# Optimization experiments

Measured on AMD Instinct MI355X. Metric: run time of the kernel, lower is better.

Reference implementation:

```python
import jax, jax.numpy as jnp
import numpy as np

EPS = 1e-10
REG = 1e-6  # regularization_weight passed to sparse_image_warp


def _phi(r2):
    # order-2 polyharmonic (thin-plate) kernel: 0.5 * r^2 * log(r^2)
    return 0.5 * r2 * jnp.log(jnp.maximum(r2, EPS))


def _tps_interpolate(train_pts, train_vals, query_pts, reg):
    # train_pts: (B,N,2), train_vals: (B,N,2), query_pts: (B,Q,2)
    b, n, _ = train_pts.shape
    d2 = jnp.sum((train_pts[:, :, None, :] - train_pts[:, None, :, :]) ** 2, -1)
    A = _phi(d2) + reg * jnp.eye(n, dtype=train_pts.dtype)  # (B,N,N)
    ones_n = jnp.ones((b, n, 1), train_pts.dtype)
    Bm = jnp.concatenate([train_pts, ones_n], -1)  # (B,N,3)
    top = jnp.concatenate([A, Bm], -1)
    bot = jnp.concatenate([jnp.swapaxes(Bm, 1, 2), jnp.zeros((b, 3, 3), train_pts.dtype)], -1)
    lhs = jnp.concatenate([top, bot], 1)  # (B,N+3,N+3)
    rhs = jnp.concatenate([train_vals, jnp.zeros((b, 3, train_vals.shape[-1]), train_vals.dtype)], 1)
    sol = jnp.linalg.solve(lhs, rhs)
    w, v = sol[:, :n], sol[:, n:]  # rbf weights (B,N,2), affine (B,3,2)
    q2 = jnp.sum((query_pts[:, :, None, :] - train_pts[:, None, :, :]) ** 2, -1)  # (B,Q,N)
    rbf = jnp.einsum('bqn,bnd->bqd', _phi(q2), w)
    ones_q = jnp.ones((b, query_pts.shape[1], 1), query_pts.dtype)
    lin = jnp.einsum('bqk,bkd->bqd', jnp.concatenate([query_pts, ones_q], -1), v)
    return rbf + lin


def _bilinear_sample(image, qy, qx):
    # image: (B,H,W,C); qy,qx: (B,Q) float query coordinates (TF dense_image_warp clamping)
    B, H, W, C = image.shape
    y0 = jnp.clip(jnp.floor(qy), 0, H - 2).astype(jnp.int32)
    x0 = jnp.clip(jnp.floor(qx), 0, W - 2).astype(jnp.int32)
    ay = jnp.clip(qy - y0.astype(qy.dtype), 0.0, 1.0)[..., None]
    ax = jnp.clip(qx - x0.astype(qx.dtype), 0.0, 1.0)[..., None]
    bi = jnp.arange(B)[:, None]
    g = lambda yi, xi: image[bi, yi, xi]  # gather -> (B,Q,C)
    top = g(y0, x0) * (1 - ax) + g(y0, x0 + 1) * ax
    bot = g(y0 + 1, x0) * (1 - ax) + g(y0 + 1, x0 + 1) * ax
    return top * (1 - ay) + bot * ay


def _sparse_image_warp(image, src, dst, reg):
    # TF semantics: flows at control points = dst - src, interpolated at dst; sample at grid - flow
    B, H, W, C = image.shape
    flows_ctrl = dst - src  # (B,N,2)
    gy, gx = jnp.meshgrid(jnp.arange(H, dtype=image.dtype), jnp.arange(W, dtype=image.dtype), indexing='ij')
    grid = jnp.broadcast_to(jnp.stack([gy, gx], -1).reshape(1, H * W, 2), (B, H * W, 2))
    dense_flow = _tps_interpolate(dst, flows_ctrl, grid, reg)  # (B,HW,2)
    query = grid - dense_flow
    warped = _bilinear_sample(image, query[..., 0], query[..., 1])
    return warped.reshape(B, H, W, C), dense_flow.reshape(B, H, W, 2)


def setup_inputs() -> dict:
    key = jax.random.key(0)
    ks = jax.random.split(key, 8)
    B, C, H, W = 16, 64, 112, 112
    n_ldmark = 16
    F = C * H * W
    x = jax.random.normal(ks[0], (B, C, H, W), jnp.float32)
    images_rendered = jax.random.normal(ks[1], (B, H, W, C), jnp.float32)
    scales = jax.random.uniform(ks[2], (B, 1), jnp.float32)
    W1 = jax.random.normal(ks[3], (128, F), jnp.float32) / np.float32(np.sqrt(F))
    b1 = jnp.zeros((128,), jnp.float32)
    W2 = jax.random.normal(ks[4], (n_ldmark * 2, 128), jnp.float32) / np.float32(np.sqrt(128))
    b2 = jnp.zeros((n_ldmark * 2,), jnp.float32)
    W3 = jax.random.normal(ks[5], (n_ldmark * 2, 128), jnp.float32) / np.float32(np.sqrt(128))
    b3 = jnp.zeros((n_ldmark * 2,), jnp.float32)
    # torch.normal(mean=0, std=50, size=(n_ldmark,2)) + [0.5*H, 0.5*W], fixed for determinism
    landmarks_mean = jax.random.normal(ks[6], (n_ldmark, 2), jnp.float32) * 50.0 \
        + jnp.array([0.5 * H, 0.5 * W], jnp.float32)
    return {"x": x, "images_rendered": images_rendered, "scales": scales,
            "W1": W1, "b1": b1, "W2": W2, "b2": b2, "W3": W3, "b3": b3,
            "landmarks_mean": landmarks_mean}


def reference(x, images_rendered, scales, W1, b1, W2, b2, W3, b3, landmarks_mean):
    B = x.shape[0]
    n_ldmark = landmarks_mean.shape[0]
    feat = x.reshape(B, -1)
    out = feat @ W1.T + b1  # (B,128)
    landmarks_pred = out @ W2.T + b2 + landmarks_mean.reshape(-1)  # (B, 2*n_ldmark)
    landmarks_disp = (out @ W3.T + b3) * scales
    # original uses .detach().clone() on landmark coords -> stop_gradient
    src = jax.lax.stop_gradient(landmarks_pred).reshape(B, n_ldmark, 2)
    dst = jax.lax.stop_gradient(landmarks_pred + landmarks_disp).reshape(B, n_ldmark, 2)
    # torch.norm(..., dim=(1,2)) = per-batch Frobenius norm, then mean
    landmarks_norm = jnp.mean(jnp.sqrt(jnp.sum((src - dst) ** 2, axis=(1, 2))))
    warped, _dense_flow = _sparse_image_warp(images_rendered, src, dst, REG)
    images_transformed = jnp.transpose(warped, (0, 3, 1, 2))  # NHWC -> NCHW
    return images_transformed, landmarks_pred, landmarks_norm
```

## Files before the change

### kernel.cpp

```cpp
#include <hip/hip_runtime.h>
#include <math.h>
#include <stdint.h>

#define F_K 802816
#define KC 1024
#define NB1 784
#define PRED_OFF 12845056
#define NORM_OFF 12845568

#define AS3 __attribute__((address_space(3)))
#define AS1 __attribute__((address_space(1)))

__device__ __forceinline__ void gload16(const float* gsrc, float* ldsbase) {
  __builtin_amdgcn_global_load_lds((const AS1 uint32_t*)gsrc, (AS3 uint32_t*)ldsbase, 16, 0, 0);
}
__device__ __forceinline__ void gload16_nt(const float* gsrc, float* ldsbase) {
  __builtin_amdgcn_global_load_lds((const AS1 uint32_t*)gsrc, (AS3 uint32_t*)ldsbase, 16, 0, 2);
}

__global__ __launch_bounds__(256) void k_gemm1(const float* __restrict__ x,
                                               const float* __restrict__ w1,
                                               float* __restrict__ part) {
  __shared__ __align__(16) float xs[256 * 4];
  __shared__ __align__(16) float ws[2048 * 4];
  const int t = threadIdx.x;
  const int wave = t >> 6, lane = t & 63;
  const int nl = t & 15;
  const int bg = (t >> 4) & 3;
  const size_t k0 = (size_t)blockIdx.x * KC;

  const float* wsrc[8];
#pragma unroll
  for (int cc = 0; cc < 8; ++cc) {
    int f = cc * 64 + lane;
    int n = f >> 2, tau = f & 3;
    int q = (tau - (n >> 1)) & 3;
    wsrc[cc] = w1 + (size_t)n * F_K + k0 + 16 * wave + 4 * q;
  }
  const float* xsrc;
  {
    int b = lane >> 2, tau = lane & 3;
    int q = (tau - (b >> 1)) & 3;
    xsrc = x + (size_t)b * F_K + k0 + 16 * wave + 4 * q;
  }
  float* xbase = xs + wave * 256;
  float* wbase = ws + wave * 2048;

  float acc[4][8];
#pragma unroll
  for (int i = 0; i < 4; ++i)
#pragma unroll
    for (int j = 0; j < 8; ++j) acc[i][j] = 0.f;

  for (int kt = 0; kt < KC / 64; ++kt) {
    asm volatile("s_waitcnt lgkmcnt(0)" ::: "memory");
    gload16(xsrc + kt * 64, xbase);
#pragma unroll
    for (int cc = 0; cc < 8; ++cc) gload16_nt(wsrc[cc] + kt * 64, wbase + cc * 256);
    asm volatile("s_waitcnt vmcnt(0)" ::: "memory");
    __builtin_amdgcn_sched_barrier(0);
#pragma unroll
    for (int q = 0; q < 4; ++q) {
      float4 xv[4];
#pragma unroll
      for (int i = 0; i < 4; ++i) {
        int b = 4 * bg + i;
        int tx = (q + (b >> 1)) & 3;
        xv[i] = *reinterpret_cast<const float4*>(&xbase[b * 16 + 4 * tx]);
      }
      const int tw = (q + (nl >> 1)) & 3;
#pragma unroll
      for (int j = 0; j < 8; ++j) {
        float4 wv = *reinterpret_cast<const float4*>(&wbase[(16 * j + nl) * 16 + 4 * tw]);
#pragma unroll
        for (int i = 0; i < 4; ++i) {
          acc[i][j] += xv[i].x * wv.x;
          acc[i][j] += xv[i].y * wv.y;
          acc[i][j] += xv[i].z * wv.z;
          acc[i][j] += xv[i].w * wv.w;
        }
      }
    }
  }

  __syncthreads();
  float* red = ws;
#pragma unroll
  for (int i = 0; i < 4; ++i)
#pragma unroll
    for (int j = 0; j < 8; ++j)
      red[wave * 2048 + (4 * bg + i) * 128 + 16 * j + nl] = acc[i][j];
  __syncthreads();
  const int o8 = t * 8;
  float4 s0 = {0, 0, 0, 0}, s1 = {0, 0, 0, 0};
#pragma unroll
  for (int w = 0; w < 4; ++w) {
    float4 a = *reinterpret_cast<const float4*>(&red[w * 2048 + o8]);
    float4 b = *reinterpret_cast<const float4*>(&red[w * 2048 + o8 + 4]);
    s0.x += a.x; s0.y += a.y; s0.z += a.z; s0.w += a.w;
    s1.x += b.x; s1.y += b.y; s1.z += b.z; s1.w += b.w;
  }
  float* pp = part + (size_t)blockIdx.x * 2048 + o8;
  *reinterpret_cast<float4*>(pp) = s0;
  *reinterpret_cast<float4*>(pp + 4) = s1;
}

__global__ __launch_bounds__(256) void k_red(const float* __restrict__ part,
                                             float* __restrict__ p2) {
  int pc = blockIdx.x >> 3, ib = blockIdx.x & 7;
  int idx = ib * 256 + threadIdx.x;
  const float* p = part + (size_t)pc * 49 * 2048 + idx;
  float s = 0.f;
  for (int q = 0; q < 49; ++q) s += p[(size_t)q * 2048];
  p2[pc * 2048 + idx] = s;
}

__global__ __launch_bounds__(64) void k_small(const float* __restrict__ p2,
    const float* __restrict__ b1, const float* __restrict__ W2, const float* __restrict__ b2,
    const float* __restrict__ W3, const float* __restrict__ b3,
    const float* __restrict__ lmean, const float* __restrict__ scales,
    float* __restrict__ dout_pred, float* __restrict__ coef, float* __restrict__ norms) {
  const int b = blockIdx.x, lane = threadIdx.x;
  __shared__ float o[128], dflat[32], fl[32], A[19][22], farr[19], sol[19][2];

  for (int h = 0; h < 2; ++h) {
    int n = lane + 64 * h;
    float s = b1[n];
    for (int pc = 0; pc < 16; ++pc) s += p2[pc * 2048 + b * 128 + n];
    o[n] = s;
  }
  __syncthreads();

  const int j = lane & 31;
  const float* Wm = (lane < 32) ? (W2 + j * 128) : (W3 + j * 128);
  float acc = 0.f;
#pragma unroll 4
  for (int n = 0; n < 128; ++n) acc += o[n] * Wm[n];
  float other = __shfl(acc, j + 32);
  float sc = scales[b];
  float dspv = 0.f;
  if (lane < 32) {
    float predv = acc + b2[j] + lmean[j];
    dspv = (other + b3[j]) * sc;
    dout_pred[b * 32 + j] = predv;
    dflat[j] = predv + dspv;
    fl[j] = dspv;
  }
  float s2 = (lane < 32) ? dspv * dspv : 0.f;
  for (int off = 32; off; off >>= 1) s2 += __shfl_xor(s2, off);
  if (lane == 0) norms[b] = sqrtf(s2);
  __syncthreads();

  for (int cell = lane; cell < 19 * 21; cell += 64) {
    int r = cell / 21, cc = cell - (cell / 21) * 21;
    float v;
    if (r < 16) {
      if (cc < 16) {
        float dy = dflat[2*r] - dflat[2*cc], dx = dflat[2*r+1] - dflat[2*cc+1];
        float d2 = dy * dy + dx * dx;
        v = 0.5f * d2 * logf(fmaxf(d2, 1e-10f));
        if (r == cc) v += 1e-6f;
      } else if (cc == 16) v = dflat[2*r];
      else if (cc == 17) v = dflat[2*r+1];
      else if (cc == 18) v = 1.0f;
      else if (cc == 19) v = fl[2*r];
      else               v = fl[2*r+1];
    } else {
      int rr = r - 16;
      if (cc < 16) v = (rr == 0) ? dflat[2*cc] : (rr == 1) ? dflat[2*cc+1] : 1.0f;
      else         v = 0.0f;
    }
    A[r][cc] = v;
  }
  __syncthreads();

  for (int k = 0; k < 19; ++k) {
    float av = (lane >= k && lane < 19) ? fabsf(A[lane][k]) : -1.0f;
    int idx = lane;
    for (int off = 32; off; off >>= 1) {
      float v2 = __shfl_xor(av, off);
      int  i2 = __shfl_xor(idx, off);
      if (v2 > av) { av = v2; idx = i2; }
    }
    idx = __shfl(idx, 0);
    if (idx != k && lane < 21) {
      float tmp = A[k][lane]; A[k][lane] = A[idx][lane]; A[idx][lane] = tmp;
    }
    __syncthreads();
    float invp = 1.0f / A[k][k];
    if (lane < 19) farr[lane] = (lane > k) ? A[lane][k] * invp : 0.0f;
    __syncthreads();
    int nr = 18 - k, nc = 20 - k;
    for (int cell = lane; cell < nr * nc; cell += 64) {
      int i = k + 1 + cell / nc, jj = k + 1 + cell % nc;
      A[i][jj] -= farr[i] * A[k][jj];
    }
    __syncthreads();
  }
  for (int k = 18; k >= 0; --k) {
    if (lane < 2) sol[k][lane] = A[k][19 + lane] / A[k][k];
    __syncthreads();
    if (lane < 2 * k) {
      int i = lane >> 1, cc = lane & 1;
      A[i][19 + cc] -= A[i][k] * sol[k][cc];
    }
    __syncthreads();
  }
  float* cf = coef + b * 80;
  if (lane < 32) { cf[lane] = sol[lane >> 1][lane & 1]; cf[38 + lane] = dflat[lane]; }
  else if (lane < 38) cf[lane] = sol[16 + ((lane - 32) >> 1)][(lane - 32) & 1];
}

__global__ __launch_bounds__(256) void k_warp(const float* __restrict__ img,
                                              const float* __restrict__ coef,
                                              const float* __restrict__ norms,
                                              float* __restrict__ out) {
  const int bid = blockIdx.x;
  const int b = bid / 112, y = bid - (bid / 112) * 112;
  const int t = threadIdx.x;
  __shared__ float qy[112], qx[112];
  __shared__ float cw[32], cv[6], cd[32];
  __shared__ float tile[64][113];

  if (bid == 0 && t == 0) {
    float s = 0.f;
    for (int i = 0; i < 16; ++i) s += norms[i];
    out[NORM_OFF] = s * (1.0f / 16.0f);
  }
  const float* cf = coef + b * 80;
  if (t < 70) {
    float v = cf[t];
    if (t < 32) cw[t] = v;
    else if (t < 38) cv[t - 32] = v;
    else cd[t - 38] = v;
  }
  __syncthreads();

  if (t < 112) {
    float fy = (float)y, fx = (float)t;
    float s0 = cv[0] * fy + cv[2] * fx + cv[4];
    float s1 = cv[1] * fy + cv[3] * fx + cv[5];
#pragma unroll
    for (int i = 0; i < 16; ++i) {
      float dy = fy - cd[2 * i], dx = fx - cd[2 * i + 1];
      float d2 = dy * dy + dx * dx;
      float ph = 0.5f * d2 * logf(fmaxf(d2, 1e-10f));
      s0 += ph * cw[2 * i];
      s1 += ph * cw[2 * i + 1];
    }
    qy[t] = fy - s0;
    qx[t] = fx - s1;
  }
  __syncthreads();

  const int wave = t >> 6, lane = t & 63;
#pragma unroll 4
  for (int p = 0; p < 28; ++p) {
    int xx = wave * 28 + p;
    float fy = qy[xx], fx = qx[xx];
    float y0f = fminf(fmaxf(floorf(fy), 0.f), 110.f);
    float x0f = fminf(fmaxf(floorf(fx), 0.f), 110.f);
    float ay = fminf(fmaxf(fy - y0f, 0.f), 1.f);
    float ax = fminf(fmaxf(fx - x0f, 0.f), 1.f);
    int y0 = (int)y0f, x0 = (int)x0f;
    const float* p00 = img + (((size_t)(b * 112 + y0) * 112 + x0) * 64) + lane;
    float v00 = p00[0], v01 = p00[64];
    float v10 = p00[112 * 64], v11 = p00[112 * 64 + 64];
    float top = v00 * (1.f - ax) + v01 * ax;
    float bot = v10 * (1.f - ax) + v11 * ax;
    tile[lane][xx] = top * (1.f - ay) + bot * ay;
  }
  __syncthreads();

  float* ob = out + (size_t)b * 64 * 12544 + y * 112;
  for (int i = 0; i < 28; ++i) {
    int idx = i * 256 + t;
    int cc = idx / 112, xx = idx - cc * 112;
    ob[(size_t)cc * 12544 + xx] = tile[cc][xx];
  }
}

extern "C" void kernel_launch(void* const* d_in, const int* in_sizes, int n_in,
                              void* d_out, int out_size, void* d_ws, size_t ws_size,
                              hipStream_t stream) {
  const float* x      = (const float*)d_in[0];
  const float* img    = (const float*)d_in[1];
  const float* scales = (const float*)d_in[2];
  const float* W1     = (const float*)d_in[3];
  const float* b1     = (const float*)d_in[4];
  const float* W2     = (const float*)d_in[5];
  const float* b2     = (const float*)d_in[6];
  const float* W3     = (const float*)d_in[7];
  const float* b3     = (const float*)d_in[8];
  const float* lmean  = (const float*)d_in[9];
  float* out = (float*)d_out;
  float* ws  = (float*)d_ws;

  float* P1   = ws;
  float* P2   = P1 + (size_t)NB1 * 2048;
  float* COEF = P2 + 16 * 2048;
  float* NORM = COEF + 16 * 80;

  k_gemm1<<<NB1, 256, 0, stream>>>(x, W1, P1);
  k_red  <<<128, 256, 0, stream>>>(P1, P2);
  k_small<<<16, 64, 0, stream>>>(P2, b1, W2, b2, W3, b3, lmean, scales,
                                 out + PRED_OFF, COEF, NORM);
  k_warp <<<16 * 112, 256, 0, stream>>>(img, COEF, NORM, out);
}
```

Baseline: 216.3 us.

## Split GEMM1 tile by output columns per wave with shared x tile and shuffle reduction

The first GEMM kernel now assigns each wave 32 output neurons across all 16 batch rows, instead of splitting K across waves. The block loads one shared 16x64 x tile, replacing per-wave x copies, and reduces partial sums across the K sub-lanes with cross-lane shuffles instead of an LDS reduction over four waves. This removes the block-level LDS reduction and the extra LDS traffic, but adds two __syncthreads per K step and drops the non-temporal load hint on W1. Per-lane reads of x from LDS become broadcast-heavy (16 float4 loads per kk step).

Result: faster. 198.6 us (-8.2%).

```diff
diff --git a/kernel.cpp b/kernel.cpp
--- a/kernel.cpp
+++ b/kernel.cpp
@@ -14,95 +14,74 @@
 __device__ __forceinline__ void gload16(const float* gsrc, float* ldsbase) {
   __builtin_amdgcn_global_load_lds((const AS1 uint32_t*)gsrc, (AS3 uint32_t*)ldsbase, 16, 0, 0);
 }
-__device__ __forceinline__ void gload16_nt(const float* gsrc, float* ldsbase) {
-  __builtin_amdgcn_global_load_lds((const AS1 uint32_t*)gsrc, (AS3 uint32_t*)ldsbase, 16, 0, 2);
-}
 
 __global__ __launch_bounds__(256) void k_gemm1(const float* __restrict__ x,
                                                const float* __restrict__ w1,
                                                float* __restrict__ part) {
-  __shared__ __align__(16) float xs[256 * 4];
-  __shared__ __align__(16) float ws[2048 * 4];
+  __shared__ __align__(16) float xs[16 * 64];
+  __shared__ __align__(16) float wsd[4 * 2048];
   const int t = threadIdx.x;
   const int wave = t >> 6, lane = t & 63;
-  const int nl = t & 15;
-  const int bg = (t >> 4) & 3;
+  const int nl = lane & 15, h = lane >> 4;
+  const int rs = lane >> 4;
+  const int ss = lane & 15;
   const size_t k0 = (size_t)blockIdx.x * KC;
 
   const float* wsrc[8];
 #pragma unroll
   for (int cc = 0; cc < 8; ++cc) {
-    int f = cc * 64 + lane;
-    int n = f >> 2, tau = f & 3;
-    int q = (tau - (n >> 1)) & 3;
-    wsrc[cc] = w1 + (size_t)n * F_K + k0 + 16 * wave + 4 * q;
-  }
-  const float* xsrc;
-  {
-    int b = lane >> 2, tau = lane & 3;
-    int q = (tau - (b >> 1)) & 3;
-    xsrc = x + (size_t)b * F_K + k0 + 16 * wave + 4 * q;
-  }
-  float* xbase = xs + wave * 256;
-  float* wbase = ws + wave * 2048;
-
-  float acc[4][8];
-#pragma unroll
-  for (int i = 0; i < 4; ++i)
-#pragma unroll
-    for (int j = 0; j < 8; ++j) acc[i][j] = 0.f;
-
+    int r = 4 * cc + rs;
+    int c = (ss - r) & 15;
+    wsrc[cc] = w1 + (size_t)(32 * wave + r) * F_K + k0 + 4 * c;
+  }
+  const float* xsrc = x + (size_t)(4 * wave + rs) * F_K + k0 + 4 * ss;
+
+  float acc[16][2];
+#pragma unroll
+  for (int b = 0; b < 16; ++b) { acc[b][0] = 0.f; acc[b][1] = 0.f; }
+
+  float* wb = wsd + wave * 2048;
   for (int kt = 0; kt < KC / 64; ++kt) {
-    asm volatile("s_waitcnt lgkmcnt(0)" ::: "memory");
-    gload16(xsrc + kt * 64, xbase);
-#pragma unroll
-    for (int cc = 0; cc < 8; ++cc) gload16_nt(wsrc[cc] + kt * 64, wbase + cc * 256);
-    asm volatile("s_waitcnt vmcnt(0)" ::: "memory");
-    __builtin_amdgcn_sched_barrier(0);
-#pragma unroll
-    for (int q = 0; q < 4; ++q) {
-      float4 xv[4];
-#pragma unroll
-      for (int i = 0; i < 4; ++i) {
-        int b = 4 * bg + i;
-        int tx = (q + (b >> 1)) & 3;
-        xv[i] = *reinterpret_cast<const float4*>(&xbase[b * 16 + 4 * tx]);
+    gload16(xsrc + kt * 64, xs + 256 * wave);
+#pragma unroll
+    for (int cc = 0; cc < 8; ++cc)
+      gload16(wsrc[cc] + kt * 64, wb + cc * 256);
+    __syncthreads();
+#pragma unroll
+    for (int kk = 0; kk < 4; ++kk) {
+      const int k4 = 4 * h + kk;
+      const int s = (k4 + nl) & 15;
+      float4 w0 = *reinterpret_cast<const float4*>(&wb[nl * 64 + 4 * s]);
+      float4 w1v = *reinterpret_cast<const float4*>(&wb[(nl + 16) * 64 + 4 * s]);
+#pragma unroll
+      for (int b = 0; b < 16; ++b) {
+        float4 xv = *reinterpret_cast<const float4*>(&xs[b * 64 + 4 * k4]);
+        acc[b][0] += xv.x * w0.x;  acc[b][0] += xv.y * w0.y;
+        acc[b][0] += xv.z * w0.z;  acc[b][0] += xv.w * w0.w;
+        acc[b][1] += xv.x * w1v.x; acc[b][1] += xv.y * w1v.y;
+        acc[b][1] += xv.z * w1v.z; acc[b][1] += xv.w * w1v.w;
       }
-      const int tw = (q + (nl >> 1)) & 3;
-#pragma unroll
-      for (int j = 0; j < 8; ++j) {
-        float4 wv = *reinterpret_cast<const float4*>(&wbase[(16 * j + nl) * 16 + 4 * tw]);
-#pragma unroll
-        for (int i = 0; i < 4; ++i) {
-          acc[i][j] += xv[i].x * wv.x;
-          acc[i][j] += xv[i].y * wv.y;
-          acc[i][j] += xv[i].z * wv.z;
-          acc[i][j] += xv[i].w * wv.w;
-        }
-      }
-    }
-  }
-
-  __syncthreads();
-  float* red = ws;
-#pragma unroll
-  for (int i = 0; i < 4; ++i)
-#pragma unroll
-    for (int j = 0; j < 8; ++j)
-      red[wave * 2048 + (4 * bg + i) * 128 + 16 * j + nl] = acc[i][j];
-  __syncthreads();
-  const int o8 = t * 8;
-  float4 s0 = {0, 0, 0, 0}, s1 = {0, 0, 0, 0};
-#pragma unroll
-  for (int w = 0; w < 4; ++w) {
-    float4 a = *reinterpret_cast<const float4*>(&red[w * 2048 + o8]);
-    float4 b = *reinterpret_cast<const float4*>(&red[w * 2048 + o8 + 4]);
-    s0.x += a.x; s0.y += a.y; s0.z += a.z; s0.w += a.w;
-    s1.x += b.x; s1.y += b.y; s1.z += b.z; s1.w += b.w;
-  }
-  float* pp = part + (size_t)blockIdx.x * 2048 + o8;
-  *reinterpret_cast<float4*>(pp) = s0;
-  *reinterpret_cast<float4*>(pp + 4) = s1;
+    }
+    __syncthreads();
+  }
+
+#pragma unroll
+  for (int b = 0; b < 16; ++b)
+#pragma unroll
+    for (int j = 0; j < 2; ++j) {
+      float v = acc[b][j];
+      v += __shfl_xor(v, 16);
+      v += __shfl_xor(v, 32);
+      acc[b][j] = v;
+    }
+  if (h == 0) {
+    float* pp = part + (size_t)blockIdx.x * 2048 + 32 * wave + nl;
+#pragma unroll
+    for (int b = 0; b < 16; ++b) {
+      pp[b * 128]      = acc[b][0];
+      pp[b * 128 + 16] = acc[b][1];
+    }
+  }
 }
 
 __global__ __launch_bounds__(256) void k_red(const float* __restrict__ part,
```
